# Kernel tuning notes

Measured on AMD Instinct MI355X. Metric: run time of the kernel, lower is better.

The kernel has to match this reference:

```python
import jax, jax.numpy as jnp
import numpy as np

M_CENTER = 3.0  # diagonal value of the 'centers' matrix
OUT_HW = (513, 513)  # original input spatial size (input_shape in torch forward)


def _conv(x, w, dilation=1, padding=0):
    return jax.lax.conv_general_dilated(
        x, w, window_strides=(1, 1),
        padding=[(padding, padding), (padding, padding)],
        rhs_dilation=(dilation, dilation),
        dimension_numbers=("NCHW", "OIHW", "NCHW"))


def _resize(x, hw):
    return jax.image.resize(x, (x.shape[0], x.shape[1], hw[0], hw[1]), method="bilinear")


def _head(low_level, out, pw, w0, w1, w2, w3, pool_w, aproj_w, cw1, cw2, cb2):
    # DeepLabHeadV3Plus (BN folded to identity at inference: gamma=1, beta=0, mean=0, var=1)
    ll = jax.nn.relu(_conv(low_level, pw))                      # [N,48,129,129]
    branches = [jax.nn.relu(_conv(out, w0))]                    # 1x1 branch
    for w, d in zip((w1, w2, w3), (6, 12, 18)):
        branches.append(jax.nn.relu(_conv(out, w, dilation=d, padding=d)))
    gp = jnp.mean(out, axis=(2, 3), keepdims=True)              # AdaptiveAvgPool2d(1)
    gp = jax.nn.relu(_conv(gp, pool_w))
    gp = jnp.broadcast_to(gp, branches[0].shape)                # bilinear upsample of 1x1 == broadcast
    branches.append(gp)
    y = jax.nn.relu(_conv(jnp.concatenate(branches, axis=1), aproj_w))  # [N,256,33,33]
    y = _resize(y, (ll.shape[2], ll.shape[3]))                  # -> 129x129
    y = jnp.concatenate([ll, y], axis=1)                        # [N,304,129,129]
    y = jax.nn.relu(_conv(y, cw1, padding=1))
    y = _conv(y, cw2) + cb2[None, :, None, None]                # [N,C,129,129]
    return y


def _forward_single(x):
    # x: [N,C,129,129] head logits. Upsample, then squared-distance to diagonal centers (m*I).
    x = _resize(x, OUT_HW)                                      # [N,C,513,513]
    C = x.shape[1]
    features_out = jnp.transpose(x, (0, 2, 3, 1))               # NHWC, as in torch
    # dist2mean[...,c] = -sum_j (f_j - m*1[j==c])^2 = -(|f|^2 - 2*m*f_c + m^2)
    sumsq = jnp.sum(x * x, axis=1, keepdims=True)
    logits = 2.0 * M_CENTER * x - sumsq - M_CENTER * M_CENTER   # [N,C,513,513]
    centers = M_CENTER * jnp.eye(C, dtype=x.dtype)
    return logits, centers, features_out


def _kaiming(key, shape):
    fan_in = shape[1] * shape[2] * shape[3]
    return jax.random.normal(key, shape, jnp.float32) * np.sqrt(2.0 / fan_in)


def _head_params(key, num_classes):
    ks = jax.random.split(key, 10)
    return dict(
        pw=_kaiming(ks[0], (48, 256, 1, 1)),
        w0=_kaiming(ks[1], (256, 2048, 1, 1)),
        w1=_kaiming(ks[2], (256, 2048, 3, 3)),
        w2=_kaiming(ks[3], (256, 2048, 3, 3)),
        w3=_kaiming(ks[4], (256, 2048, 3, 3)),
        pool_w=_kaiming(ks[5], (256, 2048, 1, 1)),
        aproj_w=_kaiming(ks[6], (256, 1280, 1, 1)),
        cw1=_kaiming(ks[7], (256, 304, 3, 3)),
        cw2=_kaiming(ks[8], (num_classes, 256, 1, 1)),
        cb2=jnp.zeros((num_classes,), jnp.float32),
    )


def setup_inputs() -> dict:
    key = jax.random.key(0)
    k_ll, k_out, k_h0, k_h1 = jax.random.split(key, 4)
    inp = {
        "low_level": jax.random.normal(k_ll, (2, 256, 129, 129), jnp.float32),
        "out": jax.random.normal(k_out, (2, 2048, 33, 33), jnp.float32),
    }
    for pref, k, nc in (("h0_", k_h0, 16), ("h1_", k_h1, 17)):
        for name, v in _head_params(k, nc).items():
            inp[pref + name] = v
    return inp


def reference(low_level, out,
              h0_pw, h0_w0, h0_w1, h0_w2, h0_w3, h0_pool_w, h0_aproj_w, h0_cw1, h0_cw2, h0_cb2,
              h1_pw, h1_w0, h1_w1, h1_w2, h1_w3, h1_pool_w, h1_aproj_w, h1_cw1, h1_cw2, h1_cb2):
    x0 = _head(low_level, out, h0_pw, h0_w0, h0_w1, h0_w2, h0_w3, h0_pool_w, h0_aproj_w, h0_cw1, h0_cw2, h0_cb2)
    x1 = _head(low_level, out, h1_pw, h1_w0, h1_w1, h1_w2, h1_w3, h1_pool_w, h1_aproj_w, h1_cw1, h1_cw2, h1_cb2)
    l0, c0, f0 = _forward_single(x0)
    l1, c1, f1 = _forward_single(x1)
    return (l0, l1, c0, c1, f0, f1)
```

## Files before the change

### kernel.cpp

```cpp
#include <hip/hip_runtime.h>

#define TPB 256

typedef _Float16 f16;
typedef __attribute__((ext_vector_type(8))) _Float16 f16x8;
typedef __attribute__((ext_vector_type(16))) float f32x16;

#define GLD_LDS(g, l) __builtin_amdgcn_global_load_lds( \
    (const __attribute__((address_space(1))) void*)(g), \
    (__attribute__((address_space(3))) void*)(l), 16, 0, 0)

__global__ __launch_bounds__(TPB)
void tcz_k(const float* __restrict__ aspp, const float* __restrict__ ll,
           f16* __restrict__ Xa, f16* __restrict__ Xll, float* __restrict__ gp)
{
    const int bid = blockIdx.x;
    const int tid = threadIdx.x;
    __shared__ float t32[32 * 33];
    __shared__ float red[4];
    if (bid >= 12816) {
        const int bc = bid - 12816;
        const float* p = aspp + (size_t)bc * 1089;
        float s = 0.f;
        for (int i = tid; i < 1089; i += TPB) s += p[i];
#pragma unroll
        for (int off = 32; off > 0; off >>= 1) s += __shfl_down(s, off, 64);
        if ((tid & 63) == 0) red[tid >> 6] = s;
        __syncthreads();
        if (tid == 0) gp[bc] = (red[0] + red[1] + red[2] + red[3]) * (1.0f / 1089.0f);
        return;
    }
    const float* src; f16* dst; int C, HW, ldk, pT, cT, bb;
    if (bid < 4480) {
        src = aspp; dst = Xa; C = 2048; HW = 1089; ldk = 2048;
        pT = bid % 35; cT = (bid / 35) % 64; bb = bid / 2240;
    } else {
        const int b2 = bid - 4480;
        src = ll; dst = Xll; C = 256; HW = 16641; ldk = 256;
        pT = b2 % 521; cT = (b2 / 521) % 8; bb = b2 / 4168;
    }
#pragma unroll
    for (int pass = 0; pass < 4; ++pass) {
        const int ch = tid / 32 + pass * 8;
        const int px = tid % 32;
        const int c = cT * 32 + ch, p = pT * 32 + px;
        float v = 0.f;
        if (c < C && p < HW) v = src[((long)bb * C + c) * HW + p];
        t32[ch * 33 + px] = v;
    }
    __syncthreads();
#pragma unroll
    for (int pass = 0; pass < 4; ++pass) {
        const int px = tid / 32 + pass * 8;
        const int ch = tid % 32;
        const int p = pT * 32 + px, c = cT * 32 + ch;
        if (p < HW && c < C)
            dst[((long)bb * HW + p) * ldk + c] = (f16)t32[ch * 33 + px];
    }
}

__global__ __launch_bounds__(TPB)
void tcr_k(const f16* __restrict__ part, f16* __restrict__ dst)
{
    __shared__ float t32[32 * 33];
    const int pT = blockIdx.x, cT = blockIdx.y, bb = blockIdx.z;
    const int tid = threadIdx.x;
    const int br = cT >> 3;
    const f16* pb = part + (long)bb * 7806464;
#pragma unroll
    for (int pass = 0; pass < 4; ++pass) {
        const int ch = tid / 32 + pass * 8;
        const int px = tid % 32;
        const int c = cT * 32 + ch;
        const int cl = c & 255;
        const int p = pT * 32 + px;
        float v = 0.f;
        if (p < 1089) {
            if (br == 0) {
                v = (float)pb[(long)cl * 1089 + p];
            } else {
                const int dl = 6 * br;
                const int s0 = 1 + 9 * (br - 1);
                const int y = p / 33;
#pragma unroll
                for (int t = 0; t < 9; ++t) {
                    const int dy = (t / 3 - 1) * dl;
                    const int yLo = max(0, -dy), yHi = min(33, 33 - dy);
                    if (y >= yLo && y < yHi)
                        v += (float)pb[((long)(s0 + t) * 256 + cl) * 1089 + p];
                }
            }
            v = fmaxf(v, 0.f);
        }
        t32[ch * 33 + px] = v;
    }
    __syncthreads();
#pragma unroll
    for (int pass = 0; pass < 4; ++pass) {
        const int px = tid / 32 + pass * 8;
        const int ch = tid % 32;
        const int p = pT * 32 + px, c = cT * 32 + ch;
        if (p < 1089)
            dst[((long)bb * 1089 + p) * 1024 + c] = (f16)t32[ch * 33 + px];
    }
}

__global__ __launch_bounds__(TPB)
void gemv1_k(const float* __restrict__ pw0, const float* __restrict__ pw1,
             const float* __restrict__ gp, float* __restrict__ gpr2)
{
    const int bh = blockIdx.x & 3;
    const int cgrp = blockIdx.x >> 2;
    const int b = bh & 1;
    const float* w = (bh >> 1) ? pw1 : pw0;
    const int c = cgrp * 16 + (threadIdx.x >> 4);
    const int kl = threadIdx.x & 15;
    const float* g = gp + (size_t)b * 2048;
    float4 acc = {0.f, 0.f, 0.f, 0.f};
    for (int k = kl * 4; k < 2048; k += 64) {
        const float4 wv = *(const float4*)&w[(size_t)c * 2048 + k];
        const float4 gv = *(const float4*)&g[k];
        acc.x = fmaf(wv.x, gv.x, acc.x);
        acc.y = fmaf(wv.y, gv.y, acc.y);
        acc.z = fmaf(wv.z, gv.z, acc.z);
        acc.w = fmaf(wv.w, gv.w, acc.w);
    }
    float s = (acc.x + acc.y) + (acc.z + acc.w);
#pragma unroll
    for (int o = 8; o; o >>= 1) s += __shfl_xor(s, o, 16);
    if (kl == 0) gpr2[bh * 256 + c] = fmaxf(s, 0.f);
}

__global__ __launch_bounds__(TPB)
void gemv2_k(const float* __restrict__ ap0, const float* __restrict__ ap1,
             const float* __restrict__ gpr2, float* __restrict__ gpc2)
{
    const int bh = blockIdx.x & 3;
    const int cgrp = blockIdx.x >> 2;
    const float* w = (bh >> 1) ? ap1 : ap0;
    const int c = cgrp * 16 + (threadIdx.x >> 4);
    const int kl = threadIdx.x & 15;
    const float* g = gpr2 + bh * 256;
    float4 acc = {0.f, 0.f, 0.f, 0.f};
    for (int k = kl * 4; k < 256; k += 64) {
        const float4 wv = *(const float4*)&w[(size_t)c * 1280 + 1024 + k];
        const float4 gv = *(const float4*)&g[k];
        acc.x = fmaf(wv.x, gv.x, acc.x);
        acc.y = fmaf(wv.y, gv.y, acc.y);
        acc.z = fmaf(wv.z, gv.z, acc.z);
        acc.w = fmaf(wv.w, gv.w, acc.w);
    }
    float s = (acc.x + acc.y) + (acc.z + acc.w);
#pragma unroll
    for (int o = 8; o; o >>= 1) s += __shfl_xor(s, o, 16);
    if (kl == 0) gpc2[bh * 256 + c] = s;
}

struct PackJob { const float* w; f16* dst; int Cout, CinUse, CinSrc, T, coP, KB, start; };
struct PackParams { PackJob j[14]; };

__global__ __launch_bounds__(TPB)
void packw_mega(PackParams P, float* __restrict__ guard)
{
    const int bid = blockIdx.x;
    const int tid = threadIdx.x;
    if (bid >= 4832) {
        float4 zv = {0.f, 0.f, 0.f, 0.f};
        float4* p = (float4*)(guard + tid * 16);
        p[0] = zv; p[1] = zv; p[2] = zv; p[3] = zv;
        return;
    }
    int ji = 0;
#pragma unroll
    for (int t = 1; t < 14; ++t) if (bid >= P.j[t].start) ji = t;
    PackJob J;
    switch (ji) {
        case 0:  J = P.j[0];  break;
        case 1:  J = P.j[1];  break;
        case 2:  J = P.j[2];  break;
        case 3:  J = P.j[3];  break;
        case 4:  J = P.j[4];  break;
        case 5:  J = P.j[5];  break;
        case 6:  J = P.j[6];  break;
        case 7:  J = P.j[7];  break;
        case 8:  J = P.j[8];  break;
        case 9:  J = P.j[9];  break;
        case 10: J = P.j[10]; break;
        case 11: J = P.j[11]; break;
        case 12: J = P.j[12]; break;
        default: J = P.j[13]; break;
    }
    const int local = bid - J.start;
    const int kb = local % J.KB;
    const int coT = local / J.KB;
    const int T = J.T;
    __shared__ float tile[16 * 577];
    const int RL = 64 * T;
    const int n = 16 * RL;
    for (int idx = tid; idx < n; idx += TPB) {
        const int row = idx / RL;
        const int jj = idx - row * RL;
        const int co = coT * 16 + row;
        const int k = kb * 64 + jj / T;
        float v = 0.f;
        if (co < J.Cout && k < J.CinUse)
            v = J.w[((long)co * J.CinSrc + kb * 64) * T + jj];
        tile[row * 577 + jj] = v;
    }
    __syncthreads();
    const int nst = 128 * T;
    for (int idx = tid; idx < nst; idx += TPB) {
        const int g = idx & 7;
        const int t = (idx >> 3) % T;
        const int co = idx / (8 * T);
        f16x8 hv;
#pragma unroll
        for (int e = 0; e < 8; ++e)
            hv[e] = (f16)tile[co * 577 + (g * 8 + e) * T + t];
        *(f16x8*)&J.dst[(((long)t * J.KB + kb) * J.coP + coT * 16 + co) * 64 + g * 8] = hv;
    }
}

__global__ __launch_bounds__(TPB, 4)
void mconv2_k(const f16* __restrict__ Xa, const f16* __restrict__ Xll,
              const f16* __restrict__ Wa, const f16* __restrict__ Wl,
              const f16* __restrict__ guard, f16* __restrict__ brp,
              f16* __restrict__ ccx)
{
    __shared__ char SH[32768];
    const int tid = threadIdx.x;

    int wg;
    {
        const int orig = blockIdx.x, nwg = gridDim.x;
        const int q = nwg >> 3, r = nwg & 7;
        const int xcd = orig & 7, off = orig >> 3;
        wg = (xcd < r ? xcd * (q + 1) : r * (q + 1) + (xcd - r) * q) + off;
    }

    const f16 *X, *Wt;
    f16* outp;
    int Cinp, W, NP, kbPerTap, coP, Cout, co0, p0, pMax, dy, dx, H, outmode;
    long ooff;
    if (wg < 2016) {
        const int mt = wg & 1;
        const int bh = (wg >> 1) & 3;
        const int z  = (wg >> 3) % 28;
        const int nt = wg / 224;
        const int b = bh & 1, hd = bh >> 1;
        Cinp = 2048; H = 33; W = 33; NP = 1089; kbPerTap = 32;
        coP = 256; Cout = 256; co0 = mt * 128;
        int br, tap;
        if (z == 0) { br = 0; tap = 0; dy = 0; dx = 0; }
        else {
            br = 1 + (z - 1) / 9; tap = (z - 1) % 9;
            const int dl = 6 * br;
            dy = (tap / 3 - 1) * dl;
            dx = (tap % 3 - 1) * dl;
        }
        const long woff = (long)hd * 14680064L +
            (br == 0 ? 0L : (br == 1 ? 524288L : (br == 2 ? 5242880L : 9961472L)));
        Wt = Wa + woff + ((long)tap * 32 * 256 + co0) * 64;
        X = Xa + (long)b * (1089L * 2048);
        const int yLo = max(0, -dy), yHi = min(33, 33 - dy);
        p0 = yLo * 33 + nt * 128;
        pMax = yHi * 33;
        if (p0 >= pMax) return;
        outp = brp;
        ooff = (long)(2 * hd + b) * 7806464L + (long)z * 278784L;
        outmode = 1;
    } else {
        const int local = wg - 2016;
        const int bh = local & 3;
        const int nt = local >> 2;
        const int b = bh & 1, hd = bh >> 1;
        Cinp = 256; H = 129; W = 129; NP = 16641; kbPerTap = 4;
        coP = 128; Cout = 48; co0 = 0;
        dy = 0; dx = 0;
        p0 = nt * 128; pMax = 16641;
        if (p0 >= pMax) return;
        X = Xll + (long)b * (16641L * 256);
        Wt = Wl + (long)hd * 32768L;
        outp = ccx;
        ooff = (long)(2 * hd + b) * 5325120L;
        outmode = 3;
    }

    const int srow = tid >> 3;
    const int sslot = tid & 7;
    int aofs[4];
#pragma unroll
    for (int q = 0; q < 4; ++q) {
        const int row = q * 32 + srow;
        aofs[q] = row * 64 + ((sslot ^ (row & 7)) << 3);
    }
    const f16* Pr[4];
#pragma unroll
    for (int q = 0; q < 4; ++q) {
        const int row = q * 32 + srow;
        const int p = p0 + row;
        bool v = p < pMax;
        const int py = v ? p / W : 0;
        const int px = v ? p - py * W : 0;
        const int sy = py + dy, sx = px + dx;
        v = v && ((unsigned)sy < (unsigned)H) && ((unsigned)sx < (unsigned)W);
        const int swz = (sslot ^ (row & 7)) << 3;
        Pr[q] = v ? (X + ((long)sy * W + sx) * Cinp + swz) : (guard + swz);
    }
    const long coStr = (long)coP * 64;

    const int lane = tid & 63, wid = tid >> 6;
    const int wm = wid >> 1, wn = wid & 1;
    const int r32 = lane & 31, hh = lane >> 5;
    const int arow0 = wm * 64 + r32, arow1 = arow0 + 32;
    const int brow0 = wn * 64 + r32, brow1 = brow0 + 32;
    const int abase0 = arow0 * 128, abase1 = arow1 * 128;
    const int bbase0 = 16384 + brow0 * 128, bbase1 = 16384 + brow1 * 128;
    const int ax0 = (arow0 & 7), ax1 = (arow1 & 7);
    const int bx0 = (brow0 & 7), bx1 = (brow1 & 7);

    f32x16 acc[2][2];
#pragma unroll
    for (int i = 0; i < 2; ++i)
#pragma unroll
        for (int j = 0; j < 2; ++j) acc[i][j] = (f32x16)(0.f);

    for (int kb = 0; kb < kbPerTap; ++kb) {
        __syncthreads();
        const f16* wsrc = Wt + (long)kb * coStr;
        const long kcol = (long)kb << 6;
        GLD_LDS(wsrc + aofs[0], SH + (tid << 4));
        GLD_LDS(wsrc + aofs[1], SH + 4096 + (tid << 4));
        GLD_LDS(wsrc + aofs[2], SH + 8192 + (tid << 4));
        GLD_LDS(wsrc + aofs[3], SH + 12288 + (tid << 4));
        GLD_LDS(Pr[0] + kcol, SH + 16384 + (tid << 4));
        GLD_LDS(Pr[1] + kcol, SH + 20480 + (tid << 4));
        GLD_LDS(Pr[2] + kcol, SH + 24576 + (tid << 4));
        GLD_LDS(Pr[3] + kcol, SH + 28672 + (tid << 4));
        __syncthreads();
        __builtin_amdgcn_s_setprio(1);
#pragma unroll
        for (int kh = 0; kh < 4; ++kh) {
            const int g = kh * 2 + hh;
            const f16x8 a0 = *(const f16x8*)(SH + abase0 + ((g ^ ax0) << 4));
            const f16x8 a1 = *(const f16x8*)(SH + abase1 + ((g ^ ax1) << 4));
            const f16x8 b0 = *(const f16x8*)(SH + bbase0 + ((g ^ bx0) << 4));
            const f16x8 b1 = *(const f16x8*)(SH + bbase1 + ((g ^ bx1) << 4));
            acc[0][0] = __builtin_amdgcn_mfma_f32_32x32x16_f16(a0, b0, acc[0][0], 0, 0, 0);
            acc[0][1] = __builtin_amdgcn_mfma_f32_32x32x16_f16(a0, b1, acc[0][1], 0, 0, 0);
            acc[1][0] = __builtin_amdgcn_mfma_f32_32x32x16_f16(a1, b0, acc[1][0], 0, 0, 0);
            acc[1][1] = __builtin_amdgcn_mfma_f32_32x32x16_f16(a1, b1, acc[1][1], 0, 0, 0);
        }
        __builtin_amdgcn_s_setprio(0);
    }

#pragma unroll
    for (int mi = 0; mi < 2; ++mi)
#pragma unroll
    for (int ni = 0; ni < 2; ++ni)
#pragma unroll
    for (int j = 0; j < 16; ++j) {
        const int m = wm * 64 + mi * 32 + 4 * hh + (j & 3) + 8 * (j >> 2);
        const int n = wn * 64 + ni * 32 + r32;
        const int co = co0 + m;
        const int p = p0 + n;
        if (co < Cout && p < pMax) {
            const float v = acc[mi][ni][j];
            if (outmode == 1)
                outp[ooff + (long)co * NP + p] = (f16)v;
            else
                outp[ooff + (long)p * 320 + co] = (f16)fmaxf(v, 0.f);
        }
    }
}

template <int OUTMODE, int RELUOUT, int BIAS>
__global__ __launch_bounds__(TPB, 4)
void mconv(const f16* __restrict__ X, const f16* __restrict__ Wp,
           const f16* __restrict__ guard, void* __restrict__ out_,
           const float* __restrict__ gpc,
           int Cinp, int Cout, int H, int W, int kss, int dl,
           int kbPerTap, int tapCnt,
           long xHstr, long wHstr, long oHstr, long outBStride,
           int coP, int ldOut, int NM, int NBH, int NZ)
{
    __shared__ char SH[32768];
    const int tid = threadIdx.x;

    int wg;
    {
        const int orig = blockIdx.x, nwg = gridDim.x;
        const int q = nwg >> 3, r = nwg & 7;
        const int xcd = orig & 7, off = orig >> 3;
        wg = (xcd < r ? xcd * (q + 1) : r * (q + 1) + (xcd - r) * q) + off;
    }
    const int mt = wg % NM; wg /= NM;
    const int bh = wg % NBH; wg /= NBH;
    const int nt = wg / NZ;
    const int b = bh & 1, hd = bh >> 1;
    const int co0 = mt * 128;
    const int NP = H * W;
    const long xBstr = (long)NP * Cinp;

    const long woff = (long)hd * wHstr, ooff = (long)hd * oHstr;
    const int p0 = nt * 128, pMax = NP;
    if (p0 >= pMax) return;
    const int half = kss >> 1;
    const int y0t = p0 / W, y1t = min(p0 + 127, pMax - 1) / W;

    int taps[9]; int nval = 0;
    for (int t = 0; t < tapCnt; ++t) {
        const int ky = t / kss;
        const int dyv = (ky - half) * dl;
        if (y1t + dyv >= 0 && y0t + dyv < H) taps[nval++] = t;
    }
    if (nval == 0) return;

    const int srow = tid >> 3;
    const int sslot = tid & 7;
    int aofs[4];
#pragma unroll
    for (int q = 0; q < 4; ++q) {
        const int row = q * 32 + srow;
        aofs[q] = row * 64 + ((sslot ^ (row & 7)) << 3);
    }
    const long coStr = (long)coP * 64;

    const int lane = tid & 63, wid = tid >> 6;
    const int wm = wid >> 1, wn = wid & 1;
    const int r32 = lane & 31, hh = lane >> 5;
    const int arow0 = wm * 64 + r32, arow1 = arow0 + 32;
    const int brow0 = wn * 64 + r32, brow1 = brow0 + 32;
    const int abase0 = arow0 * 128, abase1 = arow1 * 128;
    const int bbase0 = 16384 + brow0 * 128, bbase1 = 16384 + brow1 * 128;
    const int ax0 = (arow0 & 7), ax1 = (arow1 & 7);
    const int bx0 = (brow0 & 7), bx1 = (brow1 & 7);

    f32x16 acc[2][2];
#pragma unroll
    for (int i = 0; i < 2; ++i)
#pragma unroll
        for (int j = 0; j < 2; ++j) acc[i][j] = (f32x16)(0.f);

    const f16* Pr[4];
    for (int ti = 0; ti < nval; ++ti) {
        const int tp = taps[ti];
        const int ky = tp / kss, kx = tp - ky * kss;
        const int dy = (ky - half) * dl, dx = (kx - half) * dl;
#pragma unroll
        for (int q = 0; q < 4; ++q) {
            const int row = q * 32 + srow;
            const int p = p0 + row;
            bool v = p < pMax;
            const int py = v ? p / W : 0;
            const int px = v ? p - py * W : 0;
            const int sy = py + dy, sx = px + dx;
            v = v && ((unsigned)sy < (unsigned)H) && ((unsigned)sx < (unsigned)W);
            const int swz = (sslot ^ (row & 7)) << 3;
            Pr[q] = v ? (X + (long)b * xBstr + (long)hd * xHstr
                           + ((long)sy * W + sx) * (long)Cinp + swz)
                      : (guard + swz);
        }
        const f16* Wt = Wp + woff + ((long)tp * kbPerTap * coP + (long)co0) * 64;
        for (int kb = 0; kb < kbPerTap; ++kb) {
            __syncthreads();
            const f16* wsrc = Wt + (long)kb * coStr;
            const long kcol = (long)kb << 6;
            GLD_LDS(wsrc + aofs[0], SH + (tid << 4));
            GLD_LDS(wsrc + aofs[1], SH + 4096 + (tid << 4));
            GLD_LDS(wsrc + aofs[2], SH + 8192 + (tid << 4));
            GLD_LDS(wsrc + aofs[3], SH + 12288 + (tid << 4));
            GLD_LDS(Pr[0] + kcol, SH + 16384 + (tid << 4));
            GLD_LDS(Pr[1] + kcol, SH + 20480 + (tid << 4));
            GLD_LDS(Pr[2] + kcol, SH + 24576 + (tid << 4));
            GLD_LDS(Pr[3] + kcol, SH + 28672 + (tid << 4));
            __syncthreads();
            __builtin_amdgcn_s_setprio(1);
#pragma unroll
            for (int kh = 0; kh < 4; ++kh) {
                const int g = kh * 2 + hh;
                const f16x8 a0 = *(const f16x8*)(SH + abase0 + ((g ^ ax0) << 4));
                const f16x8 a1 = *(const f16x8*)(SH + abase1 + ((g ^ ax1) << 4));
                const f16x8 b0 = *(const f16x8*)(SH + bbase0 + ((g ^ bx0) << 4));
                const f16x8 b1 = *(const f16x8*)(SH + bbase1 + ((g ^ bx1) << 4));
                acc[0][0] = __builtin_amdgcn_mfma_f32_32x32x16_f16(a0, b0, acc[0][0], 0, 0, 0);
                acc[0][1] = __builtin_amdgcn_mfma_f32_32x32x16_f16(a0, b1, acc[0][1], 0, 0, 0);
                acc[1][0] = __builtin_amdgcn_mfma_f32_32x32x16_f16(a1, b0, acc[1][0], 0, 0, 0);
                acc[1][1] = __builtin_amdgcn_mfma_f32_32x32x16_f16(a1, b1, acc[1][1], 0, 0, 0);
            }
            __builtin_amdgcn_s_setprio(0);
        }
    }

    const long outB = (long)b * outBStride + ooff;
    const float* gpcp = BIAS ? (gpc + (long)(b + 2 * hd) * 256) : nullptr;
#pragma unroll
    for (int mi = 0; mi < 2; ++mi)
#pragma unroll
    for (int ni = 0; ni < 2; ++ni)
#pragma unroll
    for (int j = 0; j < 16; ++j) {
        const int m = wm * 64 + mi * 32 + 4 * hh + (j & 3) + 8 * (j >> 2);
        const int n = wn * 64 + ni * 32 + r32;
        const int co = co0 + m;
        const int p = p0 + n;
        if (co < Cout && p < pMax) {
            float v = acc[mi][ni][j];
            if (BIAS) v += gpcp[co];
            if (RELUOUT) v = fmaxf(v, 0.f);
            if (OUTMODE == 1) ((f16*)out_)[outB + (long)co * NP + p] = (f16)v;
            else              ((f16*)out_)[outB + (long)p * ldOut + co] = (f16)v;
        }
    }
}

__global__ __launch_bounds__(TPB)
void ups2pad_k(const f16* __restrict__ ybx, f16* __restrict__ ccx)
{
    const int idx = blockIdx.x * TPB + threadIdx.x;
    if (idx >= 4 * 16641 * 34) return;
    const int s = idx / (16641 * 34);
    const int rem = idx - s * (16641 * 34);
    const int p = rem / 34;
    const int cg = rem - p * 34;
    if (cg >= 32) {
        f16x8 zv = (f16x8)(f16)0.f;
        *(f16x8*)(ccx + ((long)s * 16641 + p) * 320 + 304 + (cg - 32) * 8) = zv;
        return;
    }
    const int oy = p / 129, ox = p % 129;
    const float sc = 33.0f / 129.0f;
    const float sx = (ox + 0.5f) * sc - 0.5f;
    const float sy = (oy + 0.5f) * sc - 0.5f;
    int ix0 = (int)floorf(sx), iy0 = (int)floorf(sy);
    const float fx = sx - ix0, fy = sy - iy0;
    int ix1 = min(32, max(0, ix0 + 1)); ix0 = min(32, max(0, ix0));
    int iy1 = min(32, max(0, iy0 + 1)); iy0 = min(32, max(0, iy0));
    const f16* base = ybx + (long)s * 1089 * 256 + cg * 8;
    const f16x8 v00 = *(const f16x8*)(base + ((long)iy0 * 33 + ix0) * 256);
    const f16x8 v01 = *(const f16x8*)(base + ((long)iy0 * 33 + ix1) * 256);
    const f16x8 v10 = *(const f16x8*)(base + ((long)iy1 * 33 + ix0) * 256);
    const f16x8 v11 = *(const f16x8*)(base + ((long)iy1 * 33 + ix1) * 256);
    f16x8 r;
#pragma unroll
    for (int e = 0; e < 8; ++e) {
        const float a0 = (float)v00[e] + ((float)v01[e] - (float)v00[e]) * fx;
        const float a1 = (float)v10[e] + ((float)v11[e] - (float)v10[e]) * fx;
        r[e] = (f16)(a0 + (a1 - a0) * fy);
    }
    *(f16x8*)(ccx + ((long)s * 16641 + p) * 320 + 48 + cg * 8) = r;
}

__global__ __launch_bounds__(TPB)
void conv1x1_m(const f16* __restrict__ c1o2,
               const float* __restrict__ w0, const float* __restrict__ w1,
               const float* __restrict__ b0, const float* __restrict__ b1,
               float* __restrict__ xb2)
{
    const int h = blockIdx.z;
    const int nc = h ? 17 : 16;
    const float* w = h ? w1 : w0;
    const float* bias = h ? b1 : b0;
    __shared__ float wsm[256 * 17];
    __shared__ float bsm[17];
    const int tid = threadIdx.x;
    for (int l = tid; l < 256 * 17; l += TPB) {
        const int k = l / 17, c = l - k * 17;
        wsm[l] = (c < nc) ? w[(size_t)c * 256 + k] : 0.f;
    }
    if (tid < nc) bsm[tid] = bias[tid];
    __syncthreads();
    const int b = blockIdx.y;
    const int p = blockIdx.x * TPB + tid;
    if (p >= 16641) return;
    const f16* inB = c1o2 + (long)h * 8520192 + (long)b * 4260096 + p;
    float acc[17];
#pragma unroll
    for (int c = 0; c < 17; ++c) acc[c] = 0.f;
    for (int k = 0; k < 256; ++k) {
        const float x = (float)inB[(size_t)k * 16641];
#pragma unroll
        for (int c = 0; c < 17; ++c) acc[c] = fmaf(wsm[k * 17 + c], x, acc[c]);
    }
    float* oB = xb2 + (h ? 532512L : 0L) + ((long)b * nc) * 16641 + p;
#pragma unroll
    for (int c = 0; c < 17; ++c)
        if (c < nc) oB[(size_t)c * 16641] = acc[c] + bsm[c];
}

__global__ __launch_bounds__(TPB)
void final_m(const float* __restrict__ xb2, float* __restrict__ o)
{
    const int idx = blockIdx.x * TPB + threadIdx.x;
    if (idx >= 2 * 526338) return;
    const int hd = idx / 526338;
    int r = idx - hd * 526338;
    const int ox = r % 513; r /= 513;
    const int oy = r % 513;
    const int b = r / 513;
    const int nc = hd ? 17 : 16;
    const long HW = 513L * 513L;
    const float sc = 129.0f / 513.0f;
    const float sx = (ox + 0.5f) * sc - 0.5f;
    const float sy = (oy + 0.5f) * sc - 0.5f;
    int ix0 = (int)floorf(sx), iy0 = (int)floorf(sy);
    const float fx = sx - ix0, fy = sy - iy0;
    int ix1 = min(128, max(0, ix0 + 1)); ix0 = min(128, max(0, ix0));
    int iy1 = min(128, max(0, iy0 + 1)); iy0 = min(128, max(0, iy0));
    const float* xb = xb2 + (hd ? 532512L : 0L) + (size_t)b * nc * 16641;
    const int i00 = iy0 * 129 + ix0, i01 = iy0 * 129 + ix1;
    const int i10 = iy1 * 129 + ix0, i11 = iy1 * 129 + ix1;
    float* logits = o + (hd ? 8421408L : 0L);
    float* feats  = o + (hd ? 25791107L : 17369699L);
    float v[17];
    float ss = 0.f;
#pragma unroll
    for (int c = 0; c < 17; ++c) {
        if (c < nc) {
            const float* s = xb + (size_t)c * 16641;
            const float a0 = s[i00] + (s[i01] - s[i00]) * fx;
            const float a1 = s[i10] + (s[i11] - s[i10]) * fx;
            const float vv = a0 + (a1 - a0) * fy;
            v[c] = vv;
            ss = fmaf(vv, vv, ss);
        }
    }
    const long pix = (long)oy * 513 + ox;
#pragma unroll
    for (int c = 0; c < 17; ++c)
        if (c < nc)
            logits[((size_t)b * nc + c) * HW + pix] = fmaf(6.f, v[c], -ss - 9.f);
    float* f = feats + ((size_t)b * HW + pix) * nc;
#pragma unroll
    for (int c = 0; c < 17; ++c)
        if (c < nc) f[c] = v[c];
}

__global__ void centers_k(float* __restrict__ c0, float* __restrict__ c1)
{
    const int t = blockIdx.x * 64 + threadIdx.x;
    if (t < 256) c0[t] = (t / 16 == t % 16) ? 3.f : 0.f;
    const int u = t - 256;
    if (u >= 0 && u < 289) c1[u] = (u / 17 == u % 17) ? 3.f : 0.f;
}

extern "C" void kernel_launch(void* const* d_in, const int* in_sizes, int n_in,
                              void* d_out, int out_size, void* d_ws, size_t ws_size,
                              hipStream_t stream)
{
    const float* low_level = (const float*)d_in[0];
    const float* aspp_in   = (const float*)d_in[1];
    float* ws = (float*)d_ws;
    float* o  = (float*)d_out;

    float* GUARDF  = ws + 0;
    f16*   GUARD   = (f16*)GUARDF;
    f16*   Apack2  = (f16*)(ws + 4096);
    f16*   C1O2    = (f16*)(ws + 4096);
    f16*   AprojP2 = (f16*)(ws + 14684160);
    f16*   Cw1P2   = (f16*)(ws + 14946304);
    f16*   LlP2    = (f16*)(ws + 15683584);
    f16*   Xa      = (f16*)(ws + 15716352);
    f16*   BRX2    = (f16*)(ws + 17946624);
    f16*   YBX2    = (f16*)(ws + 20176896);
    float* XB2     = ws + 20734464;
    float* GP      = ws + 21832770;
    float* GPC2    = ws + 21836866;
    float* GPR2    = ws + 21837890;

    f16*   CCX2    = (f16*)(o + 0);
    f16*   Xll     = (f16*)(o + 10650240);
    f16*   BRpart  = (f16*)(o + 14910336);

    const long C0o = 17369154, C1oo = 17369410;

    tcz_k<<<16912, TPB, 0, stream>>>(aspp_in, low_level, Xa, Xll, GP);
    gemv1_k<<<64, TPB, 0, stream>>>(
        (const float*)d_in[2 + 5], (const float*)d_in[2 + 10 + 5], GP, GPR2);
    gemv2_k<<<64, TPB, 0, stream>>>(
        (const float*)d_in[2 + 6], (const float*)d_in[2 + 10 + 6], GPR2, GPC2);

    PackParams P;
    int start = 0;
    for (int h = 0; h < 2; ++h) {
        const float* pw    = (const float*)d_in[2 + h * 10 + 0];
        const float* w0    = (const float*)d_in[2 + h * 10 + 1];
        const float* w1    = (const float*)d_in[2 + h * 10 + 2];
        const float* w2    = (const float*)d_in[2 + h * 10 + 3];
        const float* w3    = (const float*)d_in[2 + h * 10 + 4];
        const float* aproj = (const float*)d_in[2 + h * 10 + 6];
        const float* cw1   = (const float*)d_in[2 + h * 10 + 7];
        f16* Ap = Apack2 + (long)h * 14680064;
        const PackJob jobs[7] = {
            { w0,    Ap,                          256, 2048, 2048, 1, 256, 32, 0 },
            { w1,    Ap + 524288,                 256, 2048, 2048, 9, 256, 32, 0 },
            { w2,    Ap + 5242880,                256, 2048, 2048, 9, 256, 32, 0 },
            { w3,    Ap + 9961472,                256, 2048, 2048, 9, 256, 32, 0 },
            { aproj, AprojP2 + (long)h * 262144,  256, 1024, 1280, 1, 256, 16, 0 },
            { cw1,   Cw1P2 + (long)h * 737280,    256,  304,  304, 9, 256,  5, 0 },
            { pw,    LlP2 + (long)h * 32768,       48,  256,  256, 1, 128,  4, 0 },
        };
        for (int t = 0; t < 7; ++t) {
            P.j[h * 7 + t] = jobs[t];
            P.j[h * 7 + t].start = start;
            start += jobs[t].KB * (jobs[t].coP / 16);
        }
    }
    packw_mega<<<4833, TPB, 0, stream>>>(P, GUARDF);

    mconv2_k<<<2540, TPB, 0, stream>>>(Xa, Xll, Apack2, LlP2, GUARD, BRpart, CCX2);
    tcr_k<<<dim3(35, 32, 4), TPB, 0, stream>>>(BRpart, BRX2);
    mconv<3, 1, 1><<<72, TPB, 0, stream>>>(
        BRX2, AprojP2, GUARD, YBX2, GPC2, 1024, 256, 33, 33, 1, 1,
        16, 1, 2230272L, 262144L, 557568L, 278784L, 256, 256, 2, 4, 1);
    ups2pad_k<<<8841, TPB, 0, stream>>>(YBX2, CCX2);
    mconv<1, 1, 0><<<1048, TPB, 0, stream>>>(
        CCX2, Cw1P2, GUARD, C1O2, nullptr, 320, 256, 129, 129, 3, 1,
        5, 9, 10650240L, 737280L, 8520192L, 4260096L, 256, 0, 2, 4, 1);
    conv1x1_m<<<dim3(66, 2, 2), TPB, 0, stream>>>(C1O2,
        (const float*)d_in[2 + 8], (const float*)d_in[2 + 10 + 8],
        (const float*)d_in[2 + 9], (const float*)d_in[2 + 10 + 9], XB2);
    final_m<<<4113, TPB, 0, stream>>>(XB2, o);
    centers_k<<<9, 64, 0, stream>>>(o + C0o, o + C1oo);
}
```

Baseline: 666.1 us.

## Accumulate dilated ASPP taps per kernel row inside workgroups, shrinking partial buffers

The dilated ASPP conv kernel now has each workgroup accumulate the three taps of one kernel row in registers, where before each of the nine taps got its own workgroup. This cuts the partial-sum buffer from 28 to 10 slices per batch and head. The reduction kernel then sums 3 partials per branch instead of 9, so less half-precision data is written and read back. In exchange there are fewer workgroups (1244 vs 2540) with longer K loops, which lowers parallelism on the wide GPU. The partial buffer also moves into workspace.

```diff
diff --git a/kernel.cpp b/kernel.cpp
--- a/kernel.cpp
+++ b/kernel.cpp
@@ -66,7 +66,7 @@
     const int pT = blockIdx.x, cT = blockIdx.y, bb = blockIdx.z;
     const int tid = threadIdx.x;
     const int br = cT >> 3;
-    const f16* pb = part + (long)bb * 7806464;
+    const f16* pb = part + (long)bb * 2787840;
 #pragma unroll
     for (int pass = 0; pass < 4; ++pass) {
         const int ch = tid / 32 + pass * 8;
@@ -80,14 +80,14 @@
                 v = (float)pb[(long)cl * 1089 + p];
             } else {
                 const int dl = 6 * br;
-                const int s0 = 1 + 9 * (br - 1);
                 const int y = p / 33;
-#pragma unroll
-                for (int t = 0; t < 9; ++t) {
-                    const int dy = (t / 3 - 1) * dl;
-                    const int yLo = max(0, -dy), yHi = min(33, 33 - dy);
+                const int s0 = 1 + 3 * (br - 1);
+#pragma unroll
+                for (int g = 0; g < 3; ++g) {
+                    const int dy0 = (g - 1) * dl;
+                    const int yLo = max(0, -dy0), yHi = min(33, 33 - dy0);
                     if (y >= yLo && y < yHi)
-                        v += (float)pb[((long)(s0 + t) * 256 + cl) * 1089 + p];
+                        v += (float)pb[((long)(s0 + g) * 256 + cl) * 1089 + p];
                 }
             }
             v = fmaxf(v, 0.f);
@@ -238,53 +238,52 @@
         wg = (xcd < r ? xcd * (q + 1) : r * (q + 1) + (xcd - r) * q) + off;
     }
 
-    const f16 *X, *Wt;
+    const f16 *X, *Wbase;
     f16* outp;
-    int Cinp, W, NP, kbPerTap, coP, Cout, co0, p0, pMax, dy, dx, H, outmode;
+    int Cinp, W, H, NP, kbPerTap, coP, Cout, co0, p0, pMax, outmode;
+    int tapStart, tapCnt, kss, dl;
     long ooff;
-    if (wg < 2016) {
+    if (wg < 720) {
         const int mt = wg & 1;
         const int bh = (wg >> 1) & 3;
-        const int z  = (wg >> 3) % 28;
-        const int nt = wg / 224;
+        const int z  = (wg >> 3) % 10;
+        const int nt = wg / 80;
         const int b = bh & 1, hd = bh >> 1;
         Cinp = 2048; H = 33; W = 33; NP = 1089; kbPerTap = 32;
         coP = 256; Cout = 256; co0 = mt * 128;
-        int br, tap;
-        if (z == 0) { br = 0; tap = 0; dy = 0; dx = 0; }
-        else {
-            br = 1 + (z - 1) / 9; tap = (z - 1) % 9;
-            const int dl = 6 * br;
-            dy = (tap / 3 - 1) * dl;
-            dx = (tap % 3 - 1) * dl;
-        }
+        int br, grp;
+        if (z == 0) { br = 0; grp = 1; kss = 1; dl = 1; tapStart = 0; tapCnt = 1; }
+        else { br = 1 + (z - 1) / 3; grp = (z - 1) % 3;
+               kss = 3; dl = 6 * br; tapStart = grp * 3; tapCnt = 3; }
         const long woff = (long)hd * 14680064L +
             (br == 0 ? 0L : (br == 1 ? 524288L : (br == 2 ? 5242880L : 9961472L)));
-        Wt = Wa + woff + ((long)tap * 32 * 256 + co0) * 64;
+        Wbase = Wa + woff;
         X = Xa + (long)b * (1089L * 2048);
-        const int yLo = max(0, -dy), yHi = min(33, 33 - dy);
+        const int dy0 = (kss == 1) ? 0 : (grp - 1) * dl;
+        const int yLo = max(0, -dy0), yHi = min(33, 33 - dy0);
         p0 = yLo * 33 + nt * 128;
         pMax = yHi * 33;
         if (p0 >= pMax) return;
         outp = brp;
-        ooff = (long)(2 * hd + b) * 7806464L + (long)z * 278784L;
+        ooff = (long)(2 * hd + b) * 2787840L + (long)z * 278784L;
         outmode = 1;
     } else {
-        const int local = wg - 2016;
+        const int local = wg - 720;
         const int bh = local & 3;
         const int nt = local >> 2;
         const int b = bh & 1, hd = bh >> 1;
         Cinp = 256; H = 129; W = 129; NP = 16641; kbPerTap = 4;
         coP = 128; Cout = 48; co0 = 0;
-        dy = 0; dx = 0;
+        kss = 1; dl = 1; tapStart = 0; tapCnt = 1;
         p0 = nt * 128; pMax = 16641;
         if (p0 >= pMax) return;
         X = Xll + (long)b * (16641L * 256);
-        Wt = Wl + (long)hd * 32768L;
+        Wbase = Wl + (long)hd * 32768L;
         outp = ccx;
         ooff = (long)(2 * hd + b) * 5325120L;
         outmode = 3;
     }
+    const int half = kss >> 1;
 
     const int srow = tid >> 3;
     const int sslot = tid & 7;
@@ -293,19 +292,6 @@
     for (int q = 0; q < 4; ++q) {
         const int row = q * 32 + srow;
         aofs[q] = row * 64 + ((sslot ^ (row & 7)) << 3);
-    }
-    const f16* Pr[4];
-#pragma unroll
-    for (int q = 0; q < 4; ++q) {
-        const int row = q * 32 + srow;
-        const int p = p0 + row;
-        bool v = p < pMax;
-        const int py = v ? p / W : 0;
-        const int px = v ? p - py * W : 0;
-        const int sy = py + dy, sx = px + dx;
-        v = v && ((unsigned)sy < (unsigned)H) && ((unsigned)sx < (unsigned)W);
-        const int swz = (sslot ^ (row & 7)) << 3;
-        Pr[q] = v ? (X + ((long)sy * W + sx) * Cinp + swz) : (guard + swz);
     }
     const long coStr = (long)coP * 64;
 
@@ -325,33 +311,52 @@
 #pragma unroll
         for (int j = 0; j < 2; ++j) acc[i][j] = (f32x16)(0.f);
 
-    for (int kb = 0; kb < kbPerTap; ++kb) {
-        __syncthreads();
-        const f16* wsrc = Wt + (long)kb * coStr;
-        const long kcol = (long)kb << 6;
-        GLD_LDS(wsrc + aofs[0], SH + (tid << 4));
-        GLD_LDS(wsrc + aofs[1], SH + 4096 + (tid << 4));
-        GLD_LDS(wsrc + aofs[2], SH + 8192 + (tid << 4));
-        GLD_LDS(wsrc + aofs[3], SH + 12288 + (tid << 4));
-        GLD_LDS(Pr[0] + kcol, SH + 16384 + (tid << 4));
-        GLD_LDS(Pr[1] + kcol, SH + 20480 + (tid << 4));
-        GLD_LDS(Pr[2] + kcol, SH + 24576 + (tid << 4));
-        GLD_LDS(Pr[3] + kcol, SH + 28672 + (tid << 4));
-        __syncthreads();
-        __builtin_amdgcn_s_setprio(1);
-#pragma unroll
-        for (int kh = 0; kh < 4; ++kh) {
-            const int g = kh * 2 + hh;
-            const f16x8 a0 = *(const f16x8*)(SH + abase0 + ((g ^ ax0) << 4));
-            const f16x8 a1 = *(const f16x8*)(SH + abase1 + ((g ^ ax1) << 4));
-            const f16x8 b0 = *(const f16x8*)(SH + bbase0 + ((g ^ bx0) << 4));
-            const f16x8 b1 = *(const f16x8*)(SH + bbase1 + ((g ^ bx1) << 4));
-            acc[0][0] = __builtin_amdgcn_mfma_f32_32x32x16_f16(a0, b0, acc[0][0], 0, 0, 0);
-            acc[0][1] = __builtin_amdgcn_mfma_f32_32x32x16_f16(a0, b1, acc[0][1], 0, 0, 0);
-            acc[1][0] = __builtin_amdgcn_mfma_f32_32x32x16_f16(a1, b0, acc[1][0], 0, 0, 0);
-            acc[1][1] = __builtin_amdgcn_mfma_f32_32x32x16_f16(a1, b1, acc[1][1], 0, 0, 0);
-        }
-        __builtin_amdgcn_s_setprio(0);
+    const f16* Pr[4];
+    for (int ti = 0; ti < tapCnt; ++ti) {
+        const int tp = tapStart + ti;
+        const int ky = tp / kss, kx = tp - ky * kss;
+        const int dy = (ky - half) * dl, dx = (kx - half) * dl;
+#pragma unroll
+        for (int q = 0; q < 4; ++q) {
+            const int row = q * 32 + srow;
+            const int p = p0 + row;
+            bool v = p < pMax;
+            const int py = v ? p / W : 0;
+            const int px = v ? p - py * W : 0;
+            const int sy = py + dy, sx = px + dx;
+            v = v && ((unsigned)sy < (unsigned)H) && ((unsigned)sx < (unsigned)W);
+            const int swz = (sslot ^ (row & 7)) << 3;
+            Pr[q] = v ? (X + ((long)sy * W + sx) * Cinp + swz) : (guard + swz);
+        }
+        const f16* Wt = Wbase + ((long)tp * kbPerTap * coP + (long)co0) * 64;
+        for (int kb = 0; kb < kbPerTap; ++kb) {
+            __syncthreads();
+            const f16* wsrc = Wt + (long)kb * coStr;
+            const long kcol = (long)kb << 6;
+            GLD_LDS(wsrc + aofs[0], SH + (tid << 4));
+            GLD_LDS(wsrc + aofs[1], SH + 4096 + (tid << 4));
+            GLD_LDS(wsrc + aofs[2], SH + 8192 + (tid << 4));
+            GLD_LDS(wsrc + aofs[3], SH + 12288 + (tid << 4));
+            GLD_LDS(Pr[0] + kcol, SH + 16384 + (tid << 4));
+            GLD_LDS(Pr[1] + kcol, SH + 20480 + (tid << 4));
+            GLD_LDS(Pr[2] + kcol, SH + 24576 + (tid << 4));
+            GLD_LDS(Pr[3] + kcol, SH + 28672 + (tid << 4));
+            __syncthreads();
+            __builtin_amdgcn_s_setprio(1);
+#pragma unroll
+            for (int kh = 0; kh < 4; ++kh) {
+                const int g = kh * 2 + hh;
+                const f16x8 a0 = *(const f16x8*)(SH + abase0 + ((g ^ ax0) << 4));
+                const f16x8 a1 = *(const f16x8*)(SH + abase1 + ((g ^ ax1) << 4));
+                const f16x8 b0 = *(const f16x8*)(SH + bbase0 + ((g ^ bx0) << 4));
+                const f16x8 b1 = *(const f16x8*)(SH + bbase1 + ((g ^ bx1) << 4));
+                acc[0][0] = __builtin_amdgcn_mfma_f32_32x32x16_f16(a0, b0, acc[0][0], 0, 0, 0);
+                acc[0][1] = __builtin_amdgcn_mfma_f32_32x32x16_f16(a0, b1, acc[0][1], 0, 0, 0);
+                acc[1][0] = __builtin_amdgcn_mfma_f32_32x32x16_f16(a1, b0, acc[1][0], 0, 0, 0);
+                acc[1][1] = __builtin_amdgcn_mfma_f32_32x32x16_f16(a1, b1, acc[1][1], 0, 0, 0);
+            }
+            __builtin_amdgcn_s_setprio(0);
+        }
     }
 
 #pragma unroll
@@ -661,16 +666,16 @@
     f16*   Cw1P2   = (f16*)(ws + 14946304);
     f16*   LlP2    = (f16*)(ws + 15683584);
     f16*   Xa      = (f16*)(ws + 15716352);
-    f16*   BRX2    = (f16*)(ws + 17946624);
-    f16*   YBX2    = (f16*)(ws + 20176896);
-    float* XB2     = ws + 20734464;
-    float* GP      = ws + 21832770;
-    float* GPC2    = ws + 21836866;
-    float* GPR2    = ws + 21837890;
+    f16*   BRpart  = (f16*)(ws + 17946624);
+    f16*   BRX2    = (f16*)(ws + 23522304);
+    f16*   YBX2    = (f16*)(ws + 25752576);
+    float* XB2     = ws + 26310144;
+    float* GP      = ws + 27408450;
+    float* GPC2    = ws + 27412546;
+    float* GPR2    = ws + 27413570;
 
     f16*   CCX2    = (f16*)(o + 0);
     f16*   Xll     = (f16*)(o + 10650240);
-    f16*   BRpart  = (f16*)(o + 14910336);
 
     const long C0o = 17369154, C1oo = 17369410;
 
@@ -708,7 +713,7 @@
     }
     packw_mega<<<4833, TPB, 0, stream>>>(P, GUARDF);
 
-    mconv2_k<<<2540, TPB, 0, stream>>>(Xa, Xll, Apack2, LlP2, GUARD, BRpart, CCX2);
+    mconv2_k<<<1244, TPB, 0, stream>>>(Xa, Xll, Apack2, LlP2, GUARD, BRpart, CCX2);
     tcr_k<<<dim3(35, 32, 4), TPB, 0, stream>>>(BRpart, BRX2);
     mconv<3, 1, 1><<<72, TPB, 0, stream>>>(
         BRX2, AprojP2, GUARD, YBX2, GPC2, 1024, 256, 33, 33, 1, 1,
```

New measurement: 754.1 us. 1.13x slower.
